# Performance work log

Measured on AMD Instinct MI355X. Metric: run time of the kernel, lower is better.

The kernel has to match this reference:

```python
import jax, jax.numpy as jnp
import numpy as np

NNODES = 10000
NEDGES = 160000
NCHANNELS = 128
# Map each of the 16 spherical-harmonic components (l=0..3) to its l index:
# l=0 -> 1 comp, l=1 -> 3, l=2 -> 5, l=3 -> 7.
L_MAP = jnp.array([0, 1, 1, 1, 2, 2, 2, 2, 2, 3, 3, 3, 3, 3, 3, 3], dtype=jnp.int32)


def setup_inputs() -> dict:
    key = jax.random.key(0)
    k1, k2, k3, k4, k5 = jax.random.split(key, 5)
    node_feats = jax.random.normal(k1, (NNODES, NCHANNELS), dtype=jnp.float32)
    edge_attrs = jax.random.normal(k2, (NEDGES, 16), dtype=jnp.float32)
    tp_weights = jax.random.normal(k3, (NEDGES, 4, NCHANNELS), dtype=jnp.float32)
    sender_list = jax.random.randint(k4, (NEDGES,), 0, NNODES, dtype=jnp.int64)
    receiver_list = jnp.sort(jax.random.randint(k5, (NEDGES,), 0, NNODES, dtype=jnp.int64))
    # first occurrence of each node id in the sorted receiver list
    first_occurences = jnp.searchsorted(receiver_list, jnp.arange(NNODES, dtype=jnp.int64)).astype(jnp.int64)
    return {
        "node_feats": node_feats,
        "edge_attrs": edge_attrs,
        "tp_weights": tp_weights,
        "sender_list": sender_list,
        "receiver_list": receiver_list,
        "first_occurences": first_occurences,
    }


def reference(node_feats, edge_attrs, tp_weights, sender_list, receiver_list, first_occurences):
    nnodes = node_feats.shape[0]
    # gather sender features: [E, C]
    sender_feats = node_feats[sender_list]
    # per-edge message: out[e, lm, c] = sender_feats[e, c] * edge_attrs[e, lm] * tp_weights[e, l(lm), c]
    msgs = sender_feats[:, None, :] * edge_attrs[:, :, None] * tp_weights[:, L_MAP, :]  # [E, 16, C]
    # scatter-add into receiver nodes (first_occurences is a scheduling aid; math-wise a segment sum)
    out = jax.ops.segment_sum(msgs, receiver_list, num_segments=nnodes)  # [N, 16, C]
    return out
```

## Files before the change

kernel.cpp:

```cpp
#include <hip/hip_runtime.h>


__global__ __launch_bounds__(128)
void impt_kernel(const float* __restrict__ node_feats,
                 const float* __restrict__ edge_attrs,
                 const float* __restrict__ tp_weights,
                 const int*   __restrict__ sender_list,
                 const int*   __restrict__ first_occ,
                 float*       __restrict__ out,
                 int nnodes, int nedges)
{
    const int n = blockIdx.x;
    const int c = threadIdx.x;
    const int start = first_occ[n];
    const int end   = (n + 1 < nnodes) ? first_occ[n + 1] : nedges;

    float acc[16];
#pragma unroll
    for (int i = 0; i < 16; ++i) acc[i] = 0.0f;

    for (int e = start; e < end; ++e) {
        const int   s  = sender_list[e];
        const float sf = node_feats[(size_t)s * 128 + c];

        const float* tw = tp_weights + (size_t)e * 512 + c;
        const float p0 = sf * tw[0];
        const float p1 = sf * tw[128];
        const float p2 = sf * tw[256];
        const float p3 = sf * tw[384];

        const float4* ea4 = reinterpret_cast<const float4*>(edge_attrs + (size_t)e * 16);
        const float4 ea0 = ea4[0];
        const float4 ea1 = ea4[1];
        const float4 ea2 = ea4[2];
        const float4 ea3 = ea4[3];

        acc[0]  = fmaf(p0, ea0.x, acc[0]);
        acc[1]  = fmaf(p1, ea0.y, acc[1]);
        acc[2]  = fmaf(p1, ea0.z, acc[2]);
        acc[3]  = fmaf(p1, ea0.w, acc[3]);
        acc[4]  = fmaf(p2, ea1.x, acc[4]);
        acc[5]  = fmaf(p2, ea1.y, acc[5]);
        acc[6]  = fmaf(p2, ea1.z, acc[6]);
        acc[7]  = fmaf(p2, ea1.w, acc[7]);
        acc[8]  = fmaf(p2, ea2.x, acc[8]);
        acc[9]  = fmaf(p3, ea2.y, acc[9]);
        acc[10] = fmaf(p3, ea2.z, acc[10]);
        acc[11] = fmaf(p3, ea2.w, acc[11]);
        acc[12] = fmaf(p3, ea3.x, acc[12]);
        acc[13] = fmaf(p3, ea3.y, acc[13]);
        acc[14] = fmaf(p3, ea3.z, acc[14]);
        acc[15] = fmaf(p3, ea3.w, acc[15]);
    }

    float* o = out + (size_t)n * 2048 + c;
#pragma unroll
    for (int lm = 0; lm < 16; ++lm) o[lm * 128] = acc[lm];
}

extern "C" void kernel_launch(void* const* d_in, const int* in_sizes, int n_in,
                              void* d_out, int out_size, void* d_ws, size_t ws_size,
                              hipStream_t stream)
{
    const float* node_feats = (const float*)d_in[0];
    const float* edge_attrs = (const float*)d_in[1];
    const float* tp_weights = (const float*)d_in[2];
    const int*   sender_list = (const int*)d_in[3];
    const int*   first_occ  = (const int*)d_in[5];

    const int nnodes = in_sizes[5];
    const int nedges = in_sizes[3];

    impt_kernel<<<nnodes, 128, 0, stream>>>(node_feats, edge_attrs, tp_weights,
                                            sender_list, first_occ,
                                            (float*)d_out, nnodes, nedges);
}
```

Before: 97.39 us.

## Map one wavefront per node, split edges across half-waves with float4 channels

Each 64-lane wavefront now handles one receiver node. Each half-wave takes alternate edges, and each lane covers 4 channels through float4 loads. The partial sums are combined with a cross-half shuffle and written as vectorized float4 stores. Per-edge streams (tp_weights, edge_attrs) use nontemporal loads to avoid polluting the cache. This cuts per-edge loop iterations and instruction count, but it raises register use to 64 accumulators per thread and adds a reduction step.

```diff
diff --git a/kernel.cpp b/kernel.cpp
--- a/kernel.cpp
+++ b/kernel.cpp
@@ -1,5 +1,12 @@
 #include <hip/hip_runtime.h>
 
+
+typedef float f32x4 __attribute__((ext_vector_type(4)));
+
+__device__ __forceinline__ void fma4(f32x4& a, const f32x4 p, const float s) {
+    a.x = fmaf(p.x, s, a.x); a.y = fmaf(p.y, s, a.y);
+    a.z = fmaf(p.z, s, a.z); a.w = fmaf(p.w, s, a.w);
+}
 
 __global__ __launch_bounds__(128)
 void impt_kernel(const float* __restrict__ node_feats,
@@ -10,68 +17,101 @@
                  float*       __restrict__ out,
                  int nnodes, int nedges)
 {
-    const int n = blockIdx.x;
-    const int c = threadIdx.x;
+    const int tid  = threadIdx.x;
+    const int wv   = tid >> 6;
+    const int lane = tid & 63;
+    const int h    = lane >> 5;
+    const int j    = lane & 31;
+    const int n    = blockIdx.x * 2 + wv;
+    if (n >= nnodes) return;
+
     const int start = first_occ[n];
     const int end   = (n + 1 < nnodes) ? first_occ[n + 1] : nedges;
 
-    float acc[16];
+    f32x4 acc[16];
 #pragma unroll
-    for (int i = 0; i < 16; ++i) acc[i] = 0.0f;
+    for (int i = 0; i < 16; ++i) acc[i] = (f32x4)0.f;
 
-    for (int e = start; e < end; ++e) {
-        const int   s  = sender_list[e];
-        const float sf = node_feats[(size_t)s * 128 + c];
+    auto edge_body = [&](int ee) {
+        const int s = sender_list[ee];
+        const f32x4 sf = *reinterpret_cast<const f32x4*>(node_feats + (size_t)s * 128 + 4 * j);
 
-        const float* tw = tp_weights + (size_t)e * 512 + c;
-        const float p0 = sf * tw[0];
-        const float p1 = sf * tw[128];
-        const float p2 = sf * tw[256];
-        const float p3 = sf * tw[384];
+        const f32x4* twp = reinterpret_cast<const f32x4*>(tp_weights + (size_t)ee * 512 + 4 * j);
+        const f32x4 t0 = __builtin_nontemporal_load(twp);
+        const f32x4 t1 = __builtin_nontemporal_load(twp + 32);
+        const f32x4 t2 = __builtin_nontemporal_load(twp + 64);
+        const f32x4 t3 = __builtin_nontemporal_load(twp + 96);
 
-        const float4* ea4 = reinterpret_cast<const float4*>(edge_attrs + (size_t)e * 16);
-        const float4 ea0 = ea4[0];
-        const float4 ea1 = ea4[1];
-        const float4 ea2 = ea4[2];
-        const float4 ea3 = ea4[3];
+        const f32x4* ea4 = reinterpret_cast<const f32x4*>(edge_attrs + (size_t)ee * 16);
+        const f32x4 ea0 = __builtin_nontemporal_load(ea4);
+        const f32x4 ea1 = __builtin_nontemporal_load(ea4 + 1);
+        const f32x4 ea2 = __builtin_nontemporal_load(ea4 + 2);
+        const f32x4 ea3 = __builtin_nontemporal_load(ea4 + 3);
 
-        acc[0]  = fmaf(p0, ea0.x, acc[0]);
-        acc[1]  = fmaf(p1, ea0.y, acc[1]);
-        acc[2]  = fmaf(p1, ea0.z, acc[2]);
-        acc[3]  = fmaf(p1, ea0.w, acc[3]);
-        acc[4]  = fmaf(p2, ea1.x, acc[4]);
-        acc[5]  = fmaf(p2, ea1.y, acc[5]);
-        acc[6]  = fmaf(p2, ea1.z, acc[6]);
-        acc[7]  = fmaf(p2, ea1.w, acc[7]);
-        acc[8]  = fmaf(p2, ea2.x, acc[8]);
-        acc[9]  = fmaf(p3, ea2.y, acc[9]);
-        acc[10] = fmaf(p3, ea2.z, acc[10]);
-        acc[11] = fmaf(p3, ea2.w, acc[11]);
-        acc[12] = fmaf(p3, ea3.x, acc[12]);
-        acc[13] = fmaf(p3, ea3.y, acc[13]);
-        acc[14] = fmaf(p3, ea3.z, acc[14]);
-        acc[15] = fmaf(p3, ea3.w, acc[15]);
+        const f32x4 p0 = sf * t0;
+        const f32x4 p1 = sf * t1;
+        const f32x4 p2 = sf * t2;
+        const f32x4 p3 = sf * t3;
+
+        fma4(acc[0],  p0, ea0.x);
+        fma4(acc[1],  p1, ea0.y);
+        fma4(acc[2],  p1, ea0.z);
+        fma4(acc[3],  p1, ea0.w);
+        fma4(acc[4],  p2, ea1.x);
+        fma4(acc[5],  p2, ea1.y);
+        fma4(acc[6],  p2, ea1.z);
+        fma4(acc[7],  p2, ea1.w);
+        fma4(acc[8],  p2, ea2.x);
+        fma4(acc[9],  p3, ea2.y);
+        fma4(acc[10], p3, ea2.z);
+        fma4(acc[11], p3, ea2.w);
+        fma4(acc[12], p3, ea3.x);
+        fma4(acc[13], p3, ea3.y);
+        fma4(acc[14], p3, ea3.z);
+        fma4(acc[15], p3, ea3.w);
+    };
+
+    const int cnt    = end - start;
+    const int npairs = cnt >> 1;
+    int e = start;
+    for (int it = 0; it < npairs; ++it, e += 2) {
+        edge_body(e + h);
+    }
+    if (cnt & 1) {
+        if (h == 0) edge_body(end - 1);
     }
 
-    float* o = out + (size_t)n * 2048 + c;
 #pragma unroll
-    for (int lm = 0; lm < 16; ++lm) o[lm * 128] = acc[lm];
+    for (int i = 0; i < 16; ++i) {
+        acc[i].x += __shfl_xor(acc[i].x, 32);
+        acc[i].y += __shfl_xor(acc[i].y, 32);
+        acc[i].z += __shfl_xor(acc[i].z, 32);
+        acc[i].w += __shfl_xor(acc[i].w, 32);
+    }
+
+    float* o = out + (size_t)n * 2048 + 4 * j;
+#pragma unroll
+    for (int i = 0; i < 8; ++i) {
+        const f32x4 v = (h == 0) ? acc[2 * i] : acc[2 * i + 1];
+        *reinterpret_cast<f32x4*>(o + (size_t)(2 * i + h) * 128) = v;
+    }
 }
 
 extern "C" void kernel_launch(void* const* d_in, const int* in_sizes, int n_in,
                               void* d_out, int out_size, void* d_ws, size_t ws_size,
                               hipStream_t stream)
 {
-    const float* node_feats = (const float*)d_in[0];
-    const float* edge_attrs = (const float*)d_in[1];
-    const float* tp_weights = (const float*)d_in[2];
+    const float* node_feats  = (const float*)d_in[0];
+    const float* edge_attrs  = (const float*)d_in[1];
+    const float* tp_weights  = (const float*)d_in[2];
     const int*   sender_list = (const int*)d_in[3];
-    const int*   first_occ  = (const int*)d_in[5];
+    const int*   first_occ   = (const int*)d_in[5];
 
     const int nnodes = in_sizes[5];
     const int nedges = in_sizes[3];
 
-    impt_kernel<<<nnodes, 128, 0, stream>>>(node_feats, edge_attrs, tp_weights,
-                                            sender_list, first_occ,
-                                            (float*)d_out, nnodes, nedges);
+    const int nblocks = (nnodes + 1) / 2;
+    impt_kernel<<<nblocks, 128, 0, stream>>>(node_feats, edge_attrs, tp_weights,
+                                             sender_list, first_occ,
+                                             (float*)d_out, nnodes, nedges);
 }
```

Result: slower. 151.3 us (+55.3%).

## Assign one wavefront per node with float2 channels and prefetch sender features

Applied to the files above, without the earlier changes.

Each 64-lane wavefront now handles one receiver node, with every lane covering two channels through float2 loads and stores, and four nodes share a 256-thread block. The gather of the next edge's sender features is issued one iteration early to hide its latency. This halves the thread count per node and widens the memory accesses, cutting per-edge index and edge_attrs load overhead. In exchange each thread holds twice as many accumulator registers, and load imbalance between the four nodes in a block can leave waves idle.

```diff
diff --git a/kernel.cpp b/kernel.cpp
--- a/kernel.cpp
+++ b/kernel.cpp
@@ -1,7 +1,15 @@
 #include <hip/hip_runtime.h>
 
 
-__global__ __launch_bounds__(128)
+typedef float f32x2 __attribute__((ext_vector_type(2)));
+typedef float f32x4 __attribute__((ext_vector_type(4)));
+
+__device__ __forceinline__ void fma2(f32x2& a, const f32x2 p, const float s) {
+    a.x = fmaf(p.x, s, a.x);
+    a.y = fmaf(p.y, s, a.y);
+}
+
+__global__ __launch_bounds__(256)
 void impt_kernel(const float* __restrict__ node_feats,
                  const float* __restrict__ edge_attrs,
                  const float* __restrict__ tp_weights,
@@ -10,68 +18,91 @@
                  float*       __restrict__ out,
                  int nnodes, int nedges)
 {
-    const int n = blockIdx.x;
-    const int c = threadIdx.x;
+    const int tid  = threadIdx.x;
+    const int wv   = tid >> 6;
+    const int lane = tid & 63;
+    const int n    = blockIdx.x * 4 + wv;
+    if (n >= nnodes) return;
+
     const int start = first_occ[n];
     const int end   = (n + 1 < nnodes) ? first_occ[n + 1] : nedges;
 
-    float acc[16];
+    f32x2 acc[16];
 #pragma unroll
-    for (int i = 0; i < 16; ++i) acc[i] = 0.0f;
+    for (int i = 0; i < 16; ++i) acc[i] = (f32x2)0.f;
 
-    for (int e = start; e < end; ++e) {
-        const int   s  = sender_list[e];
-        const float sf = node_feats[(size_t)s * 128 + c];
+    const float* nf_base = node_feats + 2 * lane;
+    const float* tw_base = tp_weights + 2 * lane;
 
-        const float* tw = tp_weights + (size_t)e * 512 + c;
-        const float p0 = sf * tw[0];
-        const float p1 = sf * tw[128];
-        const float p2 = sf * tw[256];
-        const float p3 = sf * tw[384];
+    if (start < end) {
+        int s0 = sender_list[start];
+        f32x2 sf_next = *reinterpret_cast<const f32x2*>(nf_base + (size_t)s0 * 128);
 
-        const float4* ea4 = reinterpret_cast<const float4*>(edge_attrs + (size_t)e * 16);
-        const float4 ea0 = ea4[0];
-        const float4 ea1 = ea4[1];
-        const float4 ea2 = ea4[2];
-        const float4 ea3 = ea4[3];
+        for (int e = start; e < end; ++e) {
+            const f32x2 sf = sf_next;
+            if (e + 1 < end) {
+                const int s = sender_list[e + 1];
+                sf_next = *reinterpret_cast<const f32x2*>(nf_base + (size_t)s * 128);
+            }
 
-        acc[0]  = fmaf(p0, ea0.x, acc[0]);
-        acc[1]  = fmaf(p1, ea0.y, acc[1]);
-        acc[2]  = fmaf(p1, ea0.z, acc[2]);
-        acc[3]  = fmaf(p1, ea0.w, acc[3]);
-        acc[4]  = fmaf(p2, ea1.x, acc[4]);
-        acc[5]  = fmaf(p2, ea1.y, acc[5]);
-        acc[6]  = fmaf(p2, ea1.z, acc[6]);
-        acc[7]  = fmaf(p2, ea1.w, acc[7]);
-        acc[8]  = fmaf(p2, ea2.x, acc[8]);
-        acc[9]  = fmaf(p3, ea2.y, acc[9]);
-        acc[10] = fmaf(p3, ea2.z, acc[10]);
-        acc[11] = fmaf(p3, ea2.w, acc[11]);
-        acc[12] = fmaf(p3, ea3.x, acc[12]);
-        acc[13] = fmaf(p3, ea3.y, acc[13]);
-        acc[14] = fmaf(p3, ea3.z, acc[14]);
-        acc[15] = fmaf(p3, ea3.w, acc[15]);
+            const f32x2* twp = reinterpret_cast<const f32x2*>(tw_base + (size_t)e * 512);
+            const f32x2 t0 = twp[0];
+            const f32x2 t1 = twp[64];
+            const f32x2 t2 = twp[128];
+            const f32x2 t3 = twp[192];
+
+            const f32x4* ea4 = reinterpret_cast<const f32x4*>(edge_attrs + (size_t)e * 16);
+            const f32x4 ea0 = ea4[0];
+            const f32x4 ea1 = ea4[1];
+            const f32x4 ea2 = ea4[2];
+            const f32x4 ea3 = ea4[3];
+
+            const f32x2 p0 = sf * t0;
+            const f32x2 p1 = sf * t1;
+            const f32x2 p2 = sf * t2;
+            const f32x2 p3 = sf * t3;
+
+            fma2(acc[0],  p0, ea0.x);
+            fma2(acc[1],  p1, ea0.y);
+            fma2(acc[2],  p1, ea0.z);
+            fma2(acc[3],  p1, ea0.w);
+            fma2(acc[4],  p2, ea1.x);
+            fma2(acc[5],  p2, ea1.y);
+            fma2(acc[6],  p2, ea1.z);
+            fma2(acc[7],  p2, ea1.w);
+            fma2(acc[8],  p2, ea2.x);
+            fma2(acc[9],  p3, ea2.y);
+            fma2(acc[10], p3, ea2.z);
+            fma2(acc[11], p3, ea2.w);
+            fma2(acc[12], p3, ea3.x);
+            fma2(acc[13], p3, ea3.y);
+            fma2(acc[14], p3, ea3.z);
+            fma2(acc[15], p3, ea3.w);
+        }
     }
 
-    float* o = out + (size_t)n * 2048 + c;
+    float* o = out + (size_t)n * 2048 + 2 * lane;
 #pragma unroll
-    for (int lm = 0; lm < 16; ++lm) o[lm * 128] = acc[lm];
+    for (int lm = 0; lm < 16; ++lm) {
+        *reinterpret_cast<f32x2*>(o + (size_t)lm * 128) = acc[lm];
+    }
 }
 
 extern "C" void kernel_launch(void* const* d_in, const int* in_sizes, int n_in,
                               void* d_out, int out_size, void* d_ws, size_t ws_size,
                               hipStream_t stream)
 {
-    const float* node_feats = (const float*)d_in[0];
-    const float* edge_attrs = (const float*)d_in[1];
-    const float* tp_weights = (const float*)d_in[2];
+    const float* node_feats  = (const float*)d_in[0];
+    const float* edge_attrs  = (const float*)d_in[1];
+    const float* tp_weights  = (const float*)d_in[2];
     const int*   sender_list = (const int*)d_in[3];
-    const int*   first_occ  = (const int*)d_in[5];
+    const int*   first_occ   = (const int*)d_in[5];
 
     const int nnodes = in_sizes[5];
     const int nedges = in_sizes[3];
 
-    impt_kernel<<<nnodes, 128, 0, stream>>>(node_feats, edge_attrs, tp_weights,
-                                            sender_list, first_occ,
-                                            (float*)d_out, nnodes, nedges);
+    const int nblocks = (nnodes + 3) / 4;
+    impt_kernel<<<nblocks, 256, 0, stream>>>(node_feats, edge_attrs, tp_weights,
+                                             sender_list, first_occ,
+                                             (float*)d_out, nnodes, nedges);
 }
```

After: 129.4 us. +32.9%, slower.
